# Kernel optimization log

Hardware: AMD Instinct MI355X
Metric: run time of the kernel (lower is better)

Reference implementation:

```python
import jax, jax.numpy as jnp
import numpy as np

NUM_QUANTIZERS = 8
CODEBOOK_SIZE = 4096
DIM = 128
BATCH = 8
SEQ = 4096


def setup_inputs() -> dict:
    key = jax.random.key(0)
    k1, k2 = jax.random.split(key)
    x = jax.random.normal(k1, (BATCH, DIM, SEQ), dtype=jnp.float32)
    codebooks = jax.random.normal(k2, (NUM_QUANTIZERS, CODEBOOK_SIZE, DIM), dtype=jnp.float32)
    return {"x": x, "codebooks": codebooks}


def _rvq(x_bnc, codebooks):
    """Residual VQ: sequential per-stage nearest-codebook quantization.

    x_bnc: [b, n, d]; codebooks: [Q, K, d].
    Returns quantized [b, n, d], indices [b, n, Q], loss scalar.
    """
    residual = x_bnc
    quantized_out = jnp.zeros_like(x_bnc)
    all_indices = []
    all_losses = []
    Q = codebooks.shape[0]
    for q in range(Q):
        cb = codebooks[q]                                   # [K, d]
        # squared-euclidean distances: ||r||^2 - 2 r.c + ||c||^2  -> [b, n, K]
        r_sq = jnp.sum(residual * residual, axis=-1, keepdims=True)
        c_sq = jnp.sum(cb * cb, axis=-1)
        dots = jnp.einsum('bnd,kd->bnk', residual, cb)
        dist = r_sq - 2.0 * dots + c_sq
        idx = jnp.argmin(dist, axis=-1)                      # [b, n]
        quant = cb[idx]                                      # [b, n, d] gather
        # straight-through estimator (grad flows to residual, not codebook)
        quant_st = residual + jax.lax.stop_gradient(quant - residual)
        quantized_out = quantized_out + quant_st
        # commitment loss (codebook is EMA-updated, so detach the quantized side)
        all_losses.append(jnp.mean((jax.lax.stop_gradient(quant) - residual) ** 2))
        residual = residual - jax.lax.stop_gradient(quant)
        all_indices.append(idx)
    indices = jnp.stack(all_indices, axis=-1)                # [b, n, Q]
    loss = jnp.mean(jnp.stack(all_losses))
    return quantized_out, indices, loss


def reference(x, codebooks):
    # encode(): 'b c n -> b n c', quantize, 'b n c -> b c n'
    x_bnc = jnp.transpose(x, (0, 2, 1))
    quant, indices, loss = _rvq(x_bnc, codebooks)
    out = jnp.transpose(quant, (0, 2, 1))                    # [b, c, n]
    return out, indices, loss
```

## Files before the change

### kernel.cpp

```cpp
#include <hip/hip_runtime.h>

typedef _Float16 half8 __attribute__((ext_vector_type(8)));
typedef float    float4v __attribute__((ext_vector_type(4)));

#define NQ 8
#define KCODES 4096
#define DIMS 128
#define BATCH 8
#define SEQ 4096
#define ROWS (BATCH*SEQ)
#define TM 64
#define NBLK (ROWS/TM)
#define RESPAD 132
#define CANDROW 67
#define OUT_ELEMS (BATCH*DIMS*SEQ)
#define IDX_ELEMS (BATCH*SEQ*NQ)
#define LOSS_DIV (1.0f/33554432.0f)
#define FRAG_HALVES ((size_t)NQ*4*256*64*8)
#define SBIAS 384.0f
#define WIN 2.0f

__device__ __forceinline__ unsigned umax_(unsigned a, unsigned b){ return a>b?a:b; }
__device__ __forceinline__ unsigned umin_(unsigned a, unsigned b){ return a<b?a:b; }

__global__ void prep_csq(const float* __restrict__ cb, float* __restrict__ csq,
                         float* __restrict__ cinit) {
    int c = blockIdx.x * 256 + threadIdx.x;
    const float4* p = (const float4*)(cb + (size_t)c * DIMS);
    float s = 0.f;
#pragma unroll
    for (int i = 0; i < 32; ++i) {
        float4 v = p[i];
        s += v.x * v.x + v.y * v.y + v.z * v.z + v.w * v.w;
    }
    csq[c] = s;
    cinit[c] = SBIAS - 0.5f * s;
}

__global__ void prep_frags(const float* __restrict__ cb, _Float16* __restrict__ bhi,
                           float* __restrict__ loss_accum) {
    int g = blockIdx.x * 256 + threadIdx.x;
    if (g == 0) loss_accum[0] = 0.f;
    int lane = g & 63;
    int nt   = (g >> 6) & 255;
    int kb   = (g >> 14) & 3;
    int q    = g >> 16;
    int code = nt * 16 + (lane & 15);
    int k0   = kb * 32 + ((lane >> 4) * 8);
    const float* src = cb + ((size_t)q * KCODES + code) * DIMS + k0;
    float4 v0 = *(const float4*)(src);
    float4 v1 = *(const float4*)(src + 4);
    half8 h;
    h[0] = (_Float16)v0.x; h[1] = (_Float16)v0.y; h[2] = (_Float16)v0.z; h[3] = (_Float16)v0.w;
    h[4] = (_Float16)v1.x; h[5] = (_Float16)v1.y; h[6] = (_Float16)v1.z; h[7] = (_Float16)v1.w;
    *(half8*)(bhi + (size_t)g * 8) = h;
}

__device__ __forceinline__ void load_b(const _Float16* __restrict__ bq,
                                       const float* __restrict__ cinq,
                                       int nt, int lane, half8 (&bh)[4], float& cs) {
#pragma unroll
    for (int kb = 0; kb < 4; ++kb) {
        size_t off = (((size_t)kb * 256 + nt) * 64 + lane) * 8;
        bh[kb] = *(const half8*)(bq + off);
    }
    cs = cinq[nt * 16 + (lane & 15)];
}

__device__ __forceinline__ void compute_tile(int nt, int lane,
        const half8 (&ahi)[4][4], const half8 (&bh)[4], float cs,
        unsigned (&p1)[4][4], unsigned (&p2)[4][4]) {
    float4v acc[4];
#pragma unroll
    for (int mt = 0; mt < 4; ++mt) { acc[mt][0] = cs; acc[mt][1] = cs; acc[mt][2] = cs; acc[mt][3] = cs; }
    __builtin_amdgcn_s_setprio(1);
#pragma unroll
    for (int kb = 0; kb < 4; ++kb)
#pragma unroll
        for (int mt = 0; mt < 4; ++mt)
            acc[mt] = __builtin_amdgcn_mfma_f32_16x16x32_f16(ahi[mt][kb], bh[kb], acc[mt], 0, 0, 0);
    __builtin_amdgcn_s_setprio(0);
    unsigned idxv = (unsigned)(nt * 16 + (lane & 15));
#pragma unroll
    for (int mt = 0; mt < 4; ++mt)
#pragma unroll
        for (int r = 0; r < 4; ++r) {
            unsigned p  = (__float_as_uint(acc[mt][r]) & 0xFFFFF000u) | idxv;
            unsigned t1 = umin_(p1[mt][r], p);
            p1[mt][r]   = umax_(p1[mt][r], p);
            p2[mt][r]   = umax_(p2[mt][r], t1);
        }
}

__launch_bounds__(256, 2)
__global__ void rvq_main(const float* __restrict__ x, const float* __restrict__ cb,
                         const _Float16* __restrict__ bhi,
                         const float* __restrict__ csq, const float* __restrict__ cinit,
                         float* __restrict__ out, float* __restrict__ loss_accum) {
    __shared__ float    res[TM][RESPAD];
    __shared__ unsigned cand[TM][CANDROW];
    __shared__ float    fbin[TM];
    __shared__ float    red[256];

    int tid  = threadIdx.x;
    int lane = tid & 63;
    int wv   = tid >> 6;
    int r0   = blockIdx.x * TM;
    int b    = r0 >> 12;
    int n0   = r0 & (SEQ - 1);
    const float* xb = x + (size_t)b * DIMS * SEQ + n0;

    {
        int d = tid >> 1, half = (tid & 1) * 32;
        const float* src = xb + (size_t)d * SEQ + half;
#pragma unroll
        for (int t4 = 0; t4 < 8; ++t4) {
            float4 v = *(const float4*)(src + t4 * 4);
            res[half + t4 * 4 + 0][d] = v.x;
            res[half + t4 * 4 + 1][d] = v.y;
            res[half + t4 * 4 + 2][d] = v.z;
            res[half + t4 * 4 + 3][d] = v.w;
        }
    }

    float lossacc = 0.f;

    for (int q = 0; q < NQ; ++q) {
        __syncthreads();

        half8 ahi[4][4];
#pragma unroll
        for (int mt = 0; mt < 4; ++mt)
#pragma unroll
        for (int kb = 0; kb < 4; ++kb) {
            int row = mt * 16 + (lane & 15);
            int k0  = kb * 32 + (lane >> 4) * 8;
            float4 v0 = *(const float4*)&res[row][k0];
            float4 v1 = *(const float4*)&res[row][k0 + 4];
            half8 h;
            h[0] = (_Float16)v0.x; h[1] = (_Float16)v0.y; h[2] = (_Float16)v0.z; h[3] = (_Float16)v0.w;
            h[4] = (_Float16)v1.x; h[5] = (_Float16)v1.y; h[6] = (_Float16)v1.z; h[7] = (_Float16)v1.w;
            ahi[mt][kb] = h;
        }

        const _Float16* bq   = bhi + (size_t)q * (4 * 256 * 64 * 8);
        const float*    cinq = cinit + q * KCODES;
        const float*    csqq = csq + q * KCODES;

        unsigned p1[4][4], p2[4][4];
#pragma unroll
        for (int mt = 0; mt < 4; ++mt)
#pragma unroll
        for (int r = 0; r < 4; ++r) { p1[mt][r] = 0u; p2[mt][r] = 0u; }

        int ntBase = wv * 64;
        half8 bh0[4], bh1[4];
        float cs0, cs1;
        load_b(bq, cinq, ntBase, lane, bh0, cs0);

        if (wv & 1) {
            float4v accD[4];
#pragma unroll
            for (int mt = 0; mt < 4; ++mt) { accD[mt][0] = cs0; accD[mt][1] = cs0; accD[mt][2] = cs0; accD[mt][3] = cs0; }
            __builtin_amdgcn_s_setprio(1);
#pragma unroll
            for (int kb = 0; kb < 3; ++kb)
#pragma unroll
                for (int mt = 0; mt < 4; ++mt)
                    accD[mt] = __builtin_amdgcn_mfma_f32_16x16x32_f16(ahi[mt][kb], bh0[kb], accD[mt], 0, 0, 0);
            __builtin_amdgcn_s_setprio(0);
            lossacc = fmaf(0.0f, (accD[0][0] + accD[1][0]) + (accD[2][0] + accD[3][0]), lossacc);
        }

        for (int i = 0; i < 64; i += 2) {
            load_b(bq, cinq, ntBase + i + 1, lane, bh1, cs1);
            compute_tile(ntBase + i, lane, ahi, bh0, cs0, p1, p2);
            load_b(bq, cinq, ntBase + ((i + 2) & 63), lane, bh0, cs0);
            compute_tile(ntBase + i + 1, lane, ahi, bh1, cs1, p1, p2);
        }

#pragma unroll
        for (int mt = 0; mt < 4; ++mt)
#pragma unroll
        for (int r = 0; r < 4; ++r) {
            unsigned a1 = p1[mt][r], a2 = p2[mt][r];
            unsigned b1 = (unsigned)__shfl_xor((int)a1, 1, 64);
            unsigned b2 = (unsigned)__shfl_xor((int)a2, 1, 64);
            unsigned n1 = umax_(a1, b1);
            unsigned n2 = umax_(umin_(a1, b1), umax_(a2, b2));
            if ((lane & 1) == 0) {
                int row = mt * 16 + (lane >> 4) * 4 + r;
                int col = wv * 16 + ((lane & 15) >> 1) * 2;
                cand[row][col]     = n1;
                cand[row][col + 1] = n2;
            }
        }
        __syncthreads();

        {
            int row = tid >> 2, s = tid & 3;
            const unsigned* cp = &cand[row][s * 16];
            unsigned m = 0;
#pragma unroll
            for (int k = 0; k < 16; ++k) m = umax_(m, cp[k]);
            m = umax_(m, (unsigned)__shfl_xor((int)m, 1, 64));
            m = umax_(m, (unsigned)__shfl_xor((int)m, 2, 64));
            float thr = __uint_as_float(m) - WIN;
            float bk = -3.4e38f;
            int   bi = KCODES;
            const float4* rv = (const float4*)&res[row][0];
            for (int k = 0; k < 16; ++k) {
                unsigned e = cp[k];
                if (__uint_as_float(e) >= thr) {
                    int idx = (int)(e & 0xFFFu);
                    const float4* cv = (const float4*)(cb + ((size_t)q * KCODES + idx) * DIMS);
                    float acc = 0.f;
#pragma unroll
                    for (int j = 0; j < 32; ++j) {
                        float4 c4 = cv[j];
                        float4 r4 = rv[j];
                        acc = fmaf(r4.x, c4.x, acc);
                        acc = fmaf(r4.y, c4.y, acc);
                        acc = fmaf(r4.z, c4.z, acc);
                        acc = fmaf(r4.w, c4.w, acc);
                    }
                    float key = acc - 0.5f * csqq[idx];
                    if (key > bk || (key == bk && idx < bi)) { bk = key; bi = idx; }
                }
            }
#pragma unroll
            for (int mask = 1; mask <= 2; mask <<= 1) {
                float ok = __shfl_xor(bk, mask, 64);
                int   oi = __shfl_xor(bi, mask, 64);
                if (ok > bk || (ok == bk && oi < bi)) { bk = ok; bi = oi; }
            }
            if (s == 0) {
                fbin[row] = (float)bi;
                out[OUT_ELEMS + (size_t)(r0 + row) * NQ + q] = (float)bi;
            }
        }
        __syncthreads();

        {
            int row = tid >> 2, j = tid & 3;
            int bi = (int)fbin[row];
            const float* cv = cb + ((size_t)q * KCODES + bi) * DIMS + j * 32;
            float* rp = &res[row][j * 32];
#pragma unroll
            for (int t = 0; t < 8; ++t) {
                float4 c4 = *(const float4*)(cv + t * 4);
                float4 r4 = *(const float4*)(rp + t * 4);
                r4.x -= c4.x; lossacc = fmaf(r4.x, r4.x, lossacc);
                r4.y -= c4.y; lossacc = fmaf(r4.y, r4.y, lossacc);
                r4.z -= c4.z; lossacc = fmaf(r4.z, r4.z, lossacc);
                r4.w -= c4.w; lossacc = fmaf(r4.w, r4.w, lossacc);
                *(float4*)(rp + t * 4) = r4;
            }
        }
    }

    __syncthreads();
    red[tid] = lossacc;
    __syncthreads();
    for (int s = 128; s > 0; s >>= 1) {
        if (tid < s) red[tid] += red[tid + s];
        __syncthreads();
    }
    if (tid == 0) atomicAdd(loss_accum, red[0]);

    {
        int d = tid >> 1, half = (tid & 1) * 32;
        const float* src = xb + (size_t)d * SEQ + half;
        float* dst = out + (size_t)b * DIMS * SEQ + (size_t)d * SEQ + n0 + half;
#pragma unroll
        for (int t4 = 0; t4 < 8; ++t4) {
            float4 v = *(const float4*)(src + t4 * 4);
            v.x -= res[half + t4 * 4 + 0][d];
            v.y -= res[half + t4 * 4 + 1][d];
            v.z -= res[half + t4 * 4 + 2][d];
            v.w -= res[half + t4 * 4 + 3][d];
            *(float4*)(dst + t4 * 4) = v;
        }
    }
}

__global__ void finish_loss(const float* __restrict__ loss_accum, float* __restrict__ out) {
    out[OUT_ELEMS + IDX_ELEMS] = loss_accum[0] * LOSS_DIV;
}

extern "C" void kernel_launch(void* const* d_in, const int* in_sizes, int n_in,
                              void* d_out, int out_size, void* d_ws, size_t ws_size,
                              hipStream_t stream) {
    const float* x  = (const float*)d_in[0];
    const float* cb = (const float*)d_in[1];
    float* out = (float*)d_out;
    char*  ws  = (char*)d_ws;

    float*     loss_accum = (float*)ws;
    float*     csq   = (float*)(ws + 256);
    float*     cinit = (float*)(ws + 256 + 131072);
    _Float16*  bhi   = (_Float16*)(ws + 256 + 262144);

    hipLaunchKernelGGL(prep_csq,   dim3(128),  dim3(256), 0, stream, cb, csq, cinit);
    hipLaunchKernelGGL(prep_frags, dim3(2048), dim3(256), 0, stream, cb, bhi, loss_accum);
    hipLaunchKernelGGL(rvq_main,   dim3(NBLK), dim3(256), 0, stream,
                       x, cb, bhi, csq, cinit, out, loss_accum);
    hipLaunchKernelGGL(finish_loss, dim3(1), dim3(1), 0, stream, loss_accum, out);
}
```

Measured before the change: 537.7 us.

## Double block to 512 threads, splitting codebook scan across eight waves

Launches the main RVQ kernel with 8 waves per block instead of 4, so each wave scans half as many codebook tiles per stage. The candidate buffer, refinement reductions, residual update and load/store loops are re-partitioned for 8 threads per row. This aims to shorten each stage's critical path and raise latency hiding. In exchange, every wave now converts the A fragments redundantly, and the 512×2 launch bound tightens register budgets, which may cause spills.

```diff
diff --git a/kernel.cpp b/kernel.cpp
--- a/kernel.cpp
+++ b/kernel.cpp
@@ -11,8 +11,9 @@
 #define ROWS (BATCH*SEQ)
 #define TM 64
 #define NBLK (ROWS/TM)
+#define NTHREADS 512
 #define RESPAD 132
-#define CANDROW 67
+#define CANDROW 131
 #define OUT_ELEMS (BATCH*DIMS*SEQ)
 #define IDX_ELEMS (BATCH*SEQ*NQ)
 #define LOSS_DIV (1.0f/33554432.0f)
@@ -92,7 +93,7 @@
         }
 }
 
-__launch_bounds__(256, 2)
+__launch_bounds__(NTHREADS, 2)
 __global__ void rvq_main(const float* __restrict__ x, const float* __restrict__ cb,
                          const _Float16* __restrict__ bhi,
                          const float* __restrict__ csq, const float* __restrict__ cinit,
@@ -100,7 +101,7 @@
     __shared__ float    res[TM][RESPAD];
     __shared__ unsigned cand[TM][CANDROW];
     __shared__ float    fbin[TM];
-    __shared__ float    red[256];
+    __shared__ float    red[NTHREADS];
 
     int tid  = threadIdx.x;
     int lane = tid & 63;
@@ -111,15 +112,15 @@
     const float* xb = x + (size_t)b * DIMS * SEQ + n0;
 
     {
-        int d = tid >> 1, half = (tid & 1) * 32;
-        const float* src = xb + (size_t)d * SEQ + half;
-#pragma unroll
-        for (int t4 = 0; t4 < 8; ++t4) {
+        int d = tid >> 2, quarter = (tid & 3) * 16;
+        const float* src = xb + (size_t)d * SEQ + quarter;
+#pragma unroll
+        for (int t4 = 0; t4 < 4; ++t4) {
             float4 v = *(const float4*)(src + t4 * 4);
-            res[half + t4 * 4 + 0][d] = v.x;
-            res[half + t4 * 4 + 1][d] = v.y;
-            res[half + t4 * 4 + 2][d] = v.z;
-            res[half + t4 * 4 + 3][d] = v.w;
+            res[quarter + t4 * 4 + 0][d] = v.x;
+            res[quarter + t4 * 4 + 1][d] = v.y;
+            res[quarter + t4 * 4 + 2][d] = v.z;
+            res[quarter + t4 * 4 + 3][d] = v.w;
         }
     }
 
@@ -153,7 +154,7 @@
 #pragma unroll
         for (int r = 0; r < 4; ++r) { p1[mt][r] = 0u; p2[mt][r] = 0u; }
 
-        int ntBase = wv * 64;
+        int ntBase = wv * 32;
         half8 bh0[4], bh1[4];
         float cs0, cs1;
         load_b(bq, cinq, ntBase, lane, bh0, cs0);
@@ -172,10 +173,10 @@
             lossacc = fmaf(0.0f, (accD[0][0] + accD[1][0]) + (accD[2][0] + accD[3][0]), lossacc);
         }
 
-        for (int i = 0; i < 64; i += 2) {
+        for (int i = 0; i < 32; i += 2) {
             load_b(bq, cinq, ntBase + i + 1, lane, bh1, cs1);
             compute_tile(ntBase + i, lane, ahi, bh0, cs0, p1, p2);
-            load_b(bq, cinq, ntBase + ((i + 2) & 63), lane, bh0, cs0);
+            load_b(bq, cinq, ntBase + ((i + 2) & 31), lane, bh0, cs0);
             compute_tile(ntBase + i + 1, lane, ahi, bh1, cs1, p1, p2);
         }
 
@@ -198,13 +199,14 @@
         __syncthreads();
 
         {
-            int row = tid >> 2, s = tid & 3;
+            int row = tid >> 3, s = tid & 7;
             const unsigned* cp = &cand[row][s * 16];
             unsigned m = 0;
 #pragma unroll
             for (int k = 0; k < 16; ++k) m = umax_(m, cp[k]);
             m = umax_(m, (unsigned)__shfl_xor((int)m, 1, 64));
             m = umax_(m, (unsigned)__shfl_xor((int)m, 2, 64));
+            m = umax_(m, (unsigned)__shfl_xor((int)m, 4, 64));
             float thr = __uint_as_float(m) - WIN;
             float bk = -3.4e38f;
             int   bi = KCODES;
@@ -229,7 +231,7 @@
                 }
             }
 #pragma unroll
-            for (int mask = 1; mask <= 2; mask <<= 1) {
+            for (int mask = 1; mask <= 4; mask <<= 1) {
                 float ok = __shfl_xor(bk, mask, 64);
                 int   oi = __shfl_xor(bi, mask, 64);
                 if (ok > bk || (ok == bk && oi < bi)) { bk = ok; bi = oi; }
@@ -242,12 +244,12 @@
         __syncthreads();
 
         {
-            int row = tid >> 2, j = tid & 3;
+            int row = tid >> 3, j = tid & 7;
             int bi = (int)fbin[row];
-            const float* cv = cb + ((size_t)q * KCODES + bi) * DIMS + j * 32;
-            float* rp = &res[row][j * 32];
-#pragma unroll
-            for (int t = 0; t < 8; ++t) {
+            const float* cv = cb + ((size_t)q * KCODES + bi) * DIMS + j * 16;
+            float* rp = &res[row][j * 16];
+#pragma unroll
+            for (int t = 0; t < 4; ++t) {
                 float4 c4 = *(const float4*)(cv + t * 4);
                 float4 r4 = *(const float4*)(rp + t * 4);
                 r4.x -= c4.x; lossacc = fmaf(r4.x, r4.x, lossacc);
@@ -262,23 +264,23 @@
     __syncthreads();
     red[tid] = lossacc;
     __syncthreads();
-    for (int s = 128; s > 0; s >>= 1) {
+    for (int s = NTHREADS / 2; s > 0; s >>= 1) {
         if (tid < s) red[tid] += red[tid + s];
         __syncthreads();
     }
     if (tid == 0) atomicAdd(loss_accum, red[0]);
 
     {
-        int d = tid >> 1, half = (tid & 1) * 32;
-        const float* src = xb + (size_t)d * SEQ + half;
-        float* dst = out + (size_t)b * DIMS * SEQ + (size_t)d * SEQ + n0 + half;
-#pragma unroll
-        for (int t4 = 0; t4 < 8; ++t4) {
+        int d = tid >> 2, quarter = (tid & 3) * 16;
+        const float* src = xb + (size_t)d * SEQ + quarter;
+        float* dst = out + (size_t)b * DIMS * SEQ + (size_t)d * SEQ + n0 + quarter;
+#pragma unroll
+        for (int t4 = 0; t4 < 4; ++t4) {
             float4 v = *(const float4*)(src + t4 * 4);
-            v.x -= res[half + t4 * 4 + 0][d];
-            v.y -= res[half + t4 * 4 + 1][d];
-            v.z -= res[half + t4 * 4 + 2][d];
-            v.w -= res[half + t4 * 4 + 3][d];
+            v.x -= res[quarter + t4 * 4 + 0][d];
+            v.y -= res[quarter + t4 * 4 + 1][d];
+            v.z -= res[quarter + t4 * 4 + 2][d];
+            v.w -= res[quarter + t4 * 4 + 3][d];
             *(float4*)(dst + t4 * 4) = v;
         }
     }
@@ -303,7 +305,7 @@
 
     hipLaunchKernelGGL(prep_csq,   dim3(128),  dim3(256), 0, stream, cb, csq, cinit);
     hipLaunchKernelGGL(prep_frags, dim3(2048), dim3(256), 0, stream, cb, bhi, loss_accum);
-    hipLaunchKernelGGL(rvq_main,   dim3(NBLK), dim3(256), 0, stream,
+    hipLaunchKernelGGL(rvq_main,   dim3(NBLK), dim3(NTHREADS), 0, stream,
                        x, cb, bhi, csq, cinit, out, loss_accum);
     hipLaunchKernelGGL(finish_loss, dim3(1), dim3(1), 0, stream, loss_accum, out);
 }
```

New measurement: 752.7 us. 40.0% more time.

## Stage codebook fragments through LDS with async global_load_lds double buffering

Applied to the files above, without the earlier changes.

Codebook B fragments are no longer loaded from global memory into registers. Each wave now streams them into a per-wave double-buffered LDS staging area using global_load_lds, waiting on vmcnt after each tile. The c-squared bias is fetched once per 4 tiles and broadcast with a shuffle, then added after the MFMAs instead of seeding the accumulator. The candidate and reduction buffers alias the staging memory to keep the LDS footprint down, and the old dummy warm-up MFMA block is removed. The per-tile full vmcnt wait serialises each load against the compute of one tile, and the extra LDS reads may add latency.

```diff
diff --git a/kernel.cpp b/kernel.cpp
--- a/kernel.cpp
+++ b/kernel.cpp
@@ -2,6 +2,7 @@
 
 typedef _Float16 half8 __attribute__((ext_vector_type(8)));
 typedef float    float4v __attribute__((ext_vector_type(4)));
+typedef unsigned int u32;
 
 #define NQ 8
 #define KCODES 4096
@@ -16,12 +17,18 @@
 #define OUT_ELEMS (BATCH*DIMS*SEQ)
 #define IDX_ELEMS (BATCH*SEQ*NQ)
 #define LOSS_DIV (1.0f/33554432.0f)
-#define FRAG_HALVES ((size_t)NQ*4*256*64*8)
+#define FRAGQ ((size_t)4*256*64*8)
 #define SBIAS 384.0f
 #define WIN 2.0f
 
 __device__ __forceinline__ unsigned umax_(unsigned a, unsigned b){ return a>b?a:b; }
 __device__ __forceinline__ unsigned umin_(unsigned a, unsigned b){ return a<b?a:b; }
+
+__device__ __forceinline__ void gload16(const void* g, void* l) {
+    __builtin_amdgcn_global_load_lds(
+        (const __attribute__((address_space(1))) u32*)g,
+        (__attribute__((address_space(3))) u32*)l, 16, 0, 0);
+}
 
 __global__ void prep_csq(const float* __restrict__ cb, float* __restrict__ csq,
                          float* __restrict__ cinit) {
@@ -56,40 +63,54 @@
     *(half8*)(bhi + (size_t)g * 8) = h;
 }
 
-__device__ __forceinline__ void load_b(const _Float16* __restrict__ bq,
-                                       const float* __restrict__ cinq,
-                                       int nt, int lane, half8 (&bh)[4], float& cs) {
-#pragma unroll
-    for (int kb = 0; kb < 4; ++kb) {
-        size_t off = (((size_t)kb * 256 + nt) * 64 + lane) * 8;
-        bh[kb] = *(const half8*)(bq + off);
-    }
-    cs = cinq[nt * 16 + (lane & 15)];
-}
-
-__device__ __forceinline__ void compute_tile(int nt, int lane,
-        const half8 (&ahi)[4][4], const half8 (&bh)[4], float cs,
-        unsigned (&p1)[4][4], unsigned (&p2)[4][4]) {
+__device__ __forceinline__ void sub_tile(
+        int j, int t, int ntBase, int lane, int csel, float csCur,
+        const _Float16* __restrict__ bq, char* stgw,
+        const half8 (&ahi)[4][4], unsigned (&p1)[4][4], unsigned (&p2)[4][4]) {
+    int nt = ntBase + t;
+    const half8* sp = (const half8*)(stgw + ((t & 1) << 12) + (lane << 4));
+    half8 b0 = sp[0], b1 = sp[64], b2 = sp[128], b3 = sp[192];
+
+    {
+        int ntn = ntBase + ((t + 1) & 63);
+        char* dst = stgw + (((t + 1) & 1) << 12);
+#pragma unroll
+        for (int kb = 0; kb < 4; ++kb) {
+            const _Float16* g = bq + (((size_t)(kb * 256 + ntn) * 64 + lane) << 3);
+            gload16(g, dst + (kb << 10));
+        }
+    }
+
+    float csv = __shfl(csCur, j * 16 + csel, 64);
+
     float4v acc[4];
 #pragma unroll
-    for (int mt = 0; mt < 4; ++mt) { acc[mt][0] = cs; acc[mt][1] = cs; acc[mt][2] = cs; acc[mt][3] = cs; }
+    for (int mt = 0; mt < 4; ++mt) { acc[mt][0]=0.f; acc[mt][1]=0.f; acc[mt][2]=0.f; acc[mt][3]=0.f; }
     __builtin_amdgcn_s_setprio(1);
 #pragma unroll
-    for (int kb = 0; kb < 4; ++kb)
-#pragma unroll
-        for (int mt = 0; mt < 4; ++mt)
-            acc[mt] = __builtin_amdgcn_mfma_f32_16x16x32_f16(ahi[mt][kb], bh[kb], acc[mt], 0, 0, 0);
+    for (int mt = 0; mt < 4; ++mt) acc[mt] = __builtin_amdgcn_mfma_f32_16x16x32_f16(ahi[mt][0], b0, acc[mt], 0, 0, 0);
+#pragma unroll
+    for (int mt = 0; mt < 4; ++mt) acc[mt] = __builtin_amdgcn_mfma_f32_16x16x32_f16(ahi[mt][1], b1, acc[mt], 0, 0, 0);
+#pragma unroll
+    for (int mt = 0; mt < 4; ++mt) acc[mt] = __builtin_amdgcn_mfma_f32_16x16x32_f16(ahi[mt][2], b2, acc[mt], 0, 0, 0);
+#pragma unroll
+    for (int mt = 0; mt < 4; ++mt) acc[mt] = __builtin_amdgcn_mfma_f32_16x16x32_f16(ahi[mt][3], b3, acc[mt], 0, 0, 0);
     __builtin_amdgcn_s_setprio(0);
-    unsigned idxv = (unsigned)(nt * 16 + (lane & 15));
+
+    unsigned idxv = (unsigned)(nt * 16 + csel);
 #pragma unroll
     for (int mt = 0; mt < 4; ++mt)
 #pragma unroll
         for (int r = 0; r < 4; ++r) {
-            unsigned p  = (__float_as_uint(acc[mt][r]) & 0xFFFFF000u) | idxv;
+            float key = acc[mt][r] + csv;
+            unsigned p  = (__float_as_uint(key) & 0xFFFFF000u) | idxv;
             unsigned t1 = umin_(p1[mt][r], p);
             p1[mt][r]   = umax_(p1[mt][r], p);
             p2[mt][r]   = umax_(p2[mt][r], t1);
         }
+
+    asm volatile("s_waitcnt vmcnt(0)" ::: "memory");
+    __builtin_amdgcn_sched_barrier(0);
 }
 
 __launch_bounds__(256, 2)
@@ -97,14 +118,16 @@
                          const _Float16* __restrict__ bhi,
                          const float* __restrict__ csq, const float* __restrict__ cinit,
                          float* __restrict__ out, float* __restrict__ loss_accum) {
-    __shared__ float    res[TM][RESPAD];
-    __shared__ unsigned cand[TM][CANDROW];
-    __shared__ float    fbin[TM];
-    __shared__ float    red[256];
+    __shared__ float res[TM][RESPAD];
+    __shared__ __align__(16) char stg[4][8192];
+    __shared__ float fbin[TM];
+    unsigned (*cand)[CANDROW] = reinterpret_cast<unsigned (*)[CANDROW]>(&stg[0][0]);
+    float* red = reinterpret_cast<float*>(&stg[0][0] + 20480);
 
     int tid  = threadIdx.x;
     int lane = tid & 63;
     int wv   = tid >> 6;
+    int csel = lane & 15;
     int r0   = blockIdx.x * TM;
     int b    = r0 >> 12;
     int n0   = r0 & (SEQ - 1);
@@ -124,16 +147,31 @@
     }
 
     float lossacc = 0.f;
+    int ntBase = wv * 64;
+    char* stgw = &stg[wv][0];
 
     for (int q = 0; q < NQ; ++q) {
         __syncthreads();
 
+        const _Float16* bq   = bhi + (size_t)q * FRAGQ;
+        const float*    cinq = cinit + q * KCODES;
+        const float*    csqq = csq + q * KCODES;
+
+        float csCur = cinq[wv * 1024 + lane];
+        {
+#pragma unroll
+            for (int kb = 0; kb < 4; ++kb) {
+                const _Float16* g = bq + (((size_t)(kb * 256 + ntBase) * 64 + lane) << 3);
+                gload16(g, stgw + (kb << 10));
+            }
+        }
+
         half8 ahi[4][4];
 #pragma unroll
         for (int mt = 0; mt < 4; ++mt)
 #pragma unroll
         for (int kb = 0; kb < 4; ++kb) {
-            int row = mt * 16 + (lane & 15);
+            int row = mt * 16 + csel;
             int k0  = kb * 32 + (lane >> 4) * 8;
             float4 v0 = *(const float4*)&res[row][k0];
             float4 v1 = *(const float4*)&res[row][k0 + 4];
@@ -143,41 +181,25 @@
             ahi[mt][kb] = h;
         }
 
-        const _Float16* bq   = bhi + (size_t)q * (4 * 256 * 64 * 8);
-        const float*    cinq = cinit + q * KCODES;
-        const float*    csqq = csq + q * KCODES;
-
         unsigned p1[4][4], p2[4][4];
 #pragma unroll
         for (int mt = 0; mt < 4; ++mt)
 #pragma unroll
         for (int r = 0; r < 4; ++r) { p1[mt][r] = 0u; p2[mt][r] = 0u; }
 
-        int ntBase = wv * 64;
-        half8 bh0[4], bh1[4];
-        float cs0, cs1;
-        load_b(bq, cinq, ntBase, lane, bh0, cs0);
-
-        if (wv & 1) {
-            float4v accD[4];
-#pragma unroll
-            for (int mt = 0; mt < 4; ++mt) { accD[mt][0] = cs0; accD[mt][1] = cs0; accD[mt][2] = cs0; accD[mt][3] = cs0; }
-            __builtin_amdgcn_s_setprio(1);
-#pragma unroll
-            for (int kb = 0; kb < 3; ++kb)
-#pragma unroll
-                for (int mt = 0; mt < 4; ++mt)
-                    accD[mt] = __builtin_amdgcn_mfma_f32_16x16x32_f16(ahi[mt][kb], bh0[kb], accD[mt], 0, 0, 0);
-            __builtin_amdgcn_s_setprio(0);
-            lossacc = fmaf(0.0f, (accD[0][0] + accD[1][0]) + (accD[2][0] + accD[3][0]), lossacc);
-        }
-
-        for (int i = 0; i < 64; i += 2) {
-            load_b(bq, cinq, ntBase + i + 1, lane, bh1, cs1);
-            compute_tile(ntBase + i, lane, ahi, bh0, cs0, p1, p2);
-            load_b(bq, cinq, ntBase + ((i + 2) & 63), lane, bh0, cs0);
-            compute_tile(ntBase + i + 1, lane, ahi, bh1, cs1, p1, p2);
-        }
+        asm volatile("s_waitcnt vmcnt(0)" ::: "memory");
+        __builtin_amdgcn_sched_barrier(0);
+
+        for (int ii = 0; ii < 16; ++ii) {
+            float csNext = cinq[wv * 1024 + (((ii + 1) & 15) << 6) + lane];
+            sub_tile(0, ii * 4 + 0, ntBase, lane, csel, csCur, bq, stgw, ahi, p1, p2);
+            sub_tile(1, ii * 4 + 1, ntBase, lane, csel, csCur, bq, stgw, ahi, p1, p2);
+            sub_tile(2, ii * 4 + 2, ntBase, lane, csel, csCur, bq, stgw, ahi, p1, p2);
+            sub_tile(3, ii * 4 + 3, ntBase, lane, csel, csCur, bq, stgw, ahi, p1, p2);
+            csCur = csNext;
+        }
+
+        __syncthreads();
 
 #pragma unroll
         for (int mt = 0; mt < 4; ++mt)
@@ -190,7 +212,7 @@
             unsigned n2 = umax_(umin_(a1, b1), umax_(a2, b2));
             if ((lane & 1) == 0) {
                 int row = mt * 16 + (lane >> 4) * 4 + r;
-                int col = wv * 16 + ((lane & 15) >> 1) * 2;
+                int col = wv * 16 + (csel >> 1) * 2;
                 cand[row][col]     = n1;
                 cand[row][col + 1] = n2;
             }
@@ -216,9 +238,9 @@
                     const float4* cv = (const float4*)(cb + ((size_t)q * KCODES + idx) * DIMS);
                     float acc = 0.f;
 #pragma unroll
-                    for (int j = 0; j < 32; ++j) {
-                        float4 c4 = cv[j];
-                        float4 r4 = rv[j];
+                    for (int jj = 0; jj < 32; ++jj) {
+                        float4 c4 = cv[jj];
+                        float4 r4 = rv[jj];
                         acc = fmaf(r4.x, c4.x, acc);
                         acc = fmaf(r4.y, c4.y, acc);
                         acc = fmaf(r4.z, c4.z, acc);
```

New measurement: 658.0 us. +22.4%, slower.
